# Kernel optimization log

Hardware: AMD Instinct MI355X
Metric: run time of the kernel (lower is better)

## Reference

```python
import jax, jax.numpy as jnp
import numpy as np

N = 100000        # nodes
E = 1600000       # directed edges
F = 602           # Reddit num_features
D = 32            # EMBEDDING_SIZE
C = 41            # Reddit num_classes
BN_EPS = 1e-5


def setup_inputs() -> dict:
    key = jax.random.key(0)
    ks = jax.random.split(key, 24)
    def w(k, shape, fan_in):
        return jax.random.normal(k, shape, dtype=jnp.float32) * (1.0 / np.sqrt(fan_in))
    inp = {
        "x": jax.random.normal(ks[0], (N, F), dtype=jnp.float32),
        "edge_index": jax.random.randint(ks[1], (2, E), 0, N, dtype=jnp.int32),
        # lin1: F -> 2*D
        "lin1_w": w(ks[2], (F, 2 * D), F), "lin1_b": jnp.zeros((2 * D,), jnp.float32),
        # conv1 MLP: 2*D -> D -> D
        "nn1_w1": w(ks[3], (2 * D, D), 2 * D), "nn1_b1": jnp.zeros((D,), jnp.float32),
        "nn1_w2": w(ks[4], (D, D), D), "nn1_b2": jnp.zeros((D,), jnp.float32),
        "bn1_g": jnp.ones((D,), jnp.float32), "bn1_b": jnp.zeros((D,), jnp.float32),
        # conv2 MLP: D -> D -> D
        "nn2_w1": w(ks[5], (D, D), D), "nn2_b1": jnp.zeros((D,), jnp.float32),
        "nn2_w2": w(ks[6], (D, D), D), "nn2_b2": jnp.zeros((D,), jnp.float32),
        "bn2_g": jnp.ones((D,), jnp.float32), "bn2_b": jnp.zeros((D,), jnp.float32),
        # heads
        "fc1_w": w(ks[7], (D, D), D), "fc1_b": jnp.zeros((D,), jnp.float32),
        "fc2_w": w(ks[8], (D, C), D), "fc2_b": jnp.zeros((C,), jnp.float32),
    }
    return inp


def _gin_conv(x, src, dst, w1, b1, w2, b2, eps=0.0):
    # sum-aggregate neighbor features (adj_t @ x) then MLP
    agg = jax.ops.segment_sum(x[src], dst, num_segments=N)  # [N, d]
    h = (1.0 + eps) * x + agg
    h = jnp.maximum(h @ w1 + b1, 0.0) @ w2 + b2
    return h


def _batch_norm(x, gamma, beta):
    # training-mode BatchNorm1d: batch statistics, biased variance
    mu = jnp.mean(x, axis=0)
    var = jnp.mean(jnp.square(x - mu), axis=0)
    return (x - mu) * jax.lax.rsqrt(var + BN_EPS) * gamma + beta


def reference(x, edge_index, lin1_w, lin1_b,
              nn1_w1, nn1_b1, nn1_w2, nn1_b2, bn1_g, bn1_b,
              nn2_w1, nn2_b1, nn2_w2, nn2_b2, bn2_g, bn2_b,
              fc1_w, fc1_b, fc2_w, fc2_b):
    src, dst = edge_index[0], edge_index[1]
    h = x @ lin1_w + lin1_b                                  # [N, 64]
    h = _batch_norm(_gin_conv(h, src, dst, nn1_w1, nn1_b1, nn1_w2, nn1_b2), bn1_g, bn1_b)
    h = _batch_norm(_gin_conv(h, src, dst, nn2_w1, nn2_b1, nn2_w2, nn2_b2), bn2_g, bn2_b)
    h = jnp.maximum(h @ fc1_w + fc1_b, 0.0)
    return h @ fc2_w + fc2_b                                 # [N, C]
```

## Files before the change

kernel.cpp:

```cpp
#include <hip/hip_runtime.h>
#include <cstdint>

#define NN 100000
#define NE 1600000
#define FI 602
#define DD 32
#define CC 41
#define BN_EPS 1e-5f
#define KSTEPS 19

#define NPB 256
#define NB 391
#define BST 4608
#define EPT 13
#define SCB 481

typedef __attribute__((ext_vector_type(8))) short bf16x8;
typedef __attribute__((ext_vector_type(4))) float f32x4;

__device__ __forceinline__ void atomAdd(float* p, float v) {
#ifdef __HIP_PLATFORM_AMD__
  unsafeAtomicAdd(p, v);
#else
  atomicAdd(p, v);
#endif
}

__device__ __forceinline__ unsigned short f2b(float f) {
  unsigned u = __float_as_uint(f);
  unsigned r = (u + 0x7fffu + ((u >> 16) & 1u)) >> 16;
  return (unsigned short)r;
}
__device__ __forceinline__ float blo(unsigned u) { return __uint_as_float(u << 16); }
__device__ __forceinline__ float bhi(unsigned u) { return __uint_as_float(u & 0xffff0000u); }

__global__ __launch_bounds__(256) void k0_prep(
    const float* __restrict__ lin1_w, const float* __restrict__ lin1_b,
    const float* __restrict__ nn1_w1,
    unsigned short* __restrict__ Bh,
    float* __restrict__ cvec,
    float* __restrict__ stats1, float* __restrict__ stats2) {
  int o = blockIdx.x * 256 + threadIdx.x;
  if (o < KSTEPS * 32 * 32) {
    int k = o >> 5, j = o & 31;
    float s = 0.f;
    if (k < FI) {
      #pragma unroll 4
      for (int c = 0; c < 2 * DD; ++c) s = fmaf(lin1_w[k * (2 * DD) + c], nn1_w1[c * DD + j], s);
    }
    int st = k >> 5, kk = k & 31, g = kk >> 3, jj = kk & 7;
    int h = j >> 4, lane = g * 16 + (j & 15);
    int idx = ((st * 2 + h) * 64 + lane) * 8 + jj;
    Bh[idx] = f2b(s);
  }
  if (blockIdx.x == 0) {
    int t = threadIdx.x;
    if (t < DD) {
      float s = 0.f;
      for (int c = 0; c < 2 * DD; ++c) s = fmaf(lin1_b[c], nn1_w1[c * DD + t], s);
      cvec[t] = s;
    }
    if (t >= 128 && t < 192) stats1[t - 128] = 0.f;
    if (t >= 192) stats2[t - 192] = 0.f;
  }
}

__global__ __launch_bounds__(256) void kb_scatter(const int* __restrict__ ei,
                                                  int* __restrict__ bcursor,
                                                  int* __restrict__ tsrc,
                                                  unsigned char* __restrict__ tdst) {
  __shared__ int cnt[NB];
  __shared__ int wbase[NB];
  const int t = threadIdx.x;
  for (int i = t; i < NB; i += 256) cnt[i] = 0;
  __syncthreads();
  const int base = blockIdx.x * (256 * EPT);
  int s[EPT], d[EPT];
  #pragma unroll
  for (int i = 0; i < EPT; ++i) {
    int e = base + i * 256 + t;
    if (e < NE) {
      s[i] = ei[e];
      d[i] = ei[NE + e];
      atomicAdd(&cnt[d[i] >> 8], 1);
    } else {
      s[i] = -1; d[i] = -1;
    }
  }
  __syncthreads();
  for (int i = t; i < NB; i += 256) wbase[i] = atomicAdd(&bcursor[i], cnt[i]);
  __syncthreads();
  #pragma unroll
  for (int i = 0; i < EPT; ++i) {
    if (d[i] >= 0) {
      int bk = d[i] >> 8;
      int p = atomicAdd(&wbase[bk], 1);
      int gp = bk * BST + p;
      tsrc[gp] = s[i];
      tdst[gp] = (unsigned char)(d[i] & (NPB - 1));
    }
  }
}

__global__ __launch_bounds__(256) void kb_fine(const int* __restrict__ bcursor,
                                               const int* __restrict__ tsrc,
                                               const unsigned char* __restrict__ tdst,
                                               int* __restrict__ rs, int* __restrict__ re,
                                               int* __restrict__ srcidx) {
  __shared__ int deg[NPB];
  __shared__ int cur[NPB];
  __shared__ int woff[4];
  const int b = blockIdx.x, t = threadIdx.x;
  const int beg = b * BST;
  const int end = beg + bcursor[b];
  deg[t] = 0;
  __syncthreads();
  for (int i = beg + t; i < end; i += 256) atomicAdd(&deg[tdst[i]], 1);
  __syncthreads();
  int v = deg[t];
  int lane = t & 63, wave = t >> 6;
  int inc = v;
  #pragma unroll
  for (int off = 1; off < 64; off <<= 1) {
    int u = __shfl_up(inc, off);
    if (lane >= off) inc += u;
  }
  if (lane == 63) woff[wave] = inc;
  __syncthreads();
  int wadd = 0;
  for (int w = 0; w < wave; ++w) wadd += woff[w];
  int excl = wadd + inc - v;
  int gnode = b * NPB + t;
  if (gnode < NN) {
    rs[gnode] = beg + excl;
    re[gnode] = beg + excl + v;
  }
  cur[t] = beg + excl;
  __syncthreads();
  for (int i = beg + t; i < end; i += 256) {
    int p = atomicAdd(&cur[tdst[i]], 1);
    srcidx[p] = tsrc[i];
  }
}

__global__ __launch_bounds__(256) void k1_mfma(
    const float* __restrict__ x,
    const unsigned short* __restrict__ Bh,
    const float* __restrict__ cvec, unsigned short* __restrict__ zb) {
  __shared__ float part[2][64][9];
  const int tid = threadIdx.x;
  const int lane = tid & 63;
  const int w = tid >> 6;
  const int rg = w & 1;
  const int kh = w >> 1;
  const int row0 = blockIdx.x * 32 + rg * 16;
  const int g = lane >> 4;
  const int r = row0 + (lane & 15);
  const float* __restrict__ xr = x + (size_t)r * FI + g * 8;
  f32x4 acc0 = {0.f, 0.f, 0.f, 0.f};
  f32x4 acc1 = {0.f, 0.f, 0.f, 0.f};

  if (kh == 0) {
    float4 a0 = *(const float4*)&xr[0];
    float4 b0 = *(const float4*)&xr[4];
    float4 a1 = *(const float4*)&xr[32];
    float4 b1 = *(const float4*)&xr[36];
    bf16x8 f0c = *(const bf16x8*)&Bh[(size_t)lane * 8];
    bf16x8 f1c = *(const bf16x8*)&Bh[(size_t)lane * 8 + 512];
    #pragma unroll
    for (int s = 0; s < 10; ++s) {
      float4 ca = a0, cb = b0;
      a0 = a1; b0 = b1;
      if (s + 2 < 10) {
        a1 = *(const float4*)&xr[(s + 2) * 32];
        b1 = *(const float4*)&xr[(s + 2) * 32 + 4];
      }
      bf16x8 f0n, f1n;
      if (s + 1 < 10) {
        const size_t fb = ((size_t)((s + 1) * 2) * 64 + lane) * 8;
        f0n = *(const bf16x8*)&Bh[fb];
        f1n = *(const bf16x8*)&Bh[fb + 512];
      }
      bf16x8 ahi, alo;
      float cv0[8] = {ca.x, ca.y, ca.z, ca.w, cb.x, cb.y, cb.z, cb.w};
      #pragma unroll
      for (int j = 0; j < 8; ++j) {
        unsigned ub = __float_as_uint(cv0[j]);
        unsigned short h = (unsigned short)(ub >> 16);
        float hv = __uint_as_float(ub & 0xffff0000u);
        float d = cv0[j] - hv;
        ahi[j] = (short)h;
        alo[j] = (short)(__float_as_uint(d) >> 16);
      }
      acc0 = __builtin_amdgcn_mfma_f32_16x16x32_bf16(ahi, f0c, acc0, 0, 0, 0);
      acc1 = __builtin_amdgcn_mfma_f32_16x16x32_bf16(ahi, f1c, acc1, 0, 0, 0);
      acc0 = __builtin_amdgcn_mfma_f32_16x16x32_bf16(alo, f0c, acc0, 0, 0, 0);
      acc1 = __builtin_amdgcn_mfma_f32_16x16x32_bf16(alo, f1c, acc1, 0, 0, 0);
      if (s + 1 < 10) { f0c = f0n; f1c = f1n; }
    }
  } else {
    float4 a0 = *(const float4*)&xr[10 * 32];
    float4 b0 = *(const float4*)&xr[10 * 32 + 4];
    float4 a1 = *(const float4*)&xr[11 * 32];
    float4 b1 = *(const float4*)&xr[11 * 32 + 4];
    bf16x8 f0c = *(const bf16x8*)&Bh[((size_t)(10 * 2) * 64 + lane) * 8];
    bf16x8 f1c = *(const bf16x8*)&Bh[((size_t)(10 * 2) * 64 + lane) * 8 + 512];
    #pragma unroll
    for (int s = 10; s < KSTEPS; ++s) {
      float4 ca = a0, cb = b0;
      a0 = a1; b0 = b1;
      if (s + 2 < KSTEPS - 1) {
        a1 = *(const float4*)&xr[(s + 2) * 32];
        b1 = *(const float4*)&xr[(s + 2) * 32 + 4];
      } else if (s + 2 == KSTEPS - 1) {
        if (g == 3) {
          float2 tt = *(const float2*)&xr[18 * 32];
          a1 = make_float4(tt.x, tt.y, 0.f, 0.f);
          b1 = make_float4(0.f, 0.f, 0.f, 0.f);
        } else {
          a1 = *(const float4*)&xr[18 * 32];
          b1 = *(const float4*)&xr[18 * 32 + 4];
        }
      }
      bf16x8 f0n, f1n;
      if (s + 1 < KSTEPS) {
        const size_t fb = ((size_t)((s + 1) * 2) * 64 + lane) * 8;
        f0n = *(const bf16x8*)&Bh[fb];
        f1n = *(const bf16x8*)&Bh[fb + 512];
      }
      bf16x8 ahi, alo;
      float cv0[8] = {ca.x, ca.y, ca.z, ca.w, cb.x, cb.y, cb.z, cb.w};
      #pragma unroll
      for (int j = 0; j < 8; ++j) {
        unsigned ub = __float_as_uint(cv0[j]);
        unsigned short h = (unsigned short)(ub >> 16);
        float hv = __uint_as_float(ub & 0xffff0000u);
        float d = cv0[j] - hv;
        ahi[j] = (short)h;
        alo[j] = (short)(__float_as_uint(d) >> 16);
      }
      acc0 = __builtin_amdgcn_mfma_f32_16x16x32_bf16(ahi, f0c, acc0, 0, 0, 0);
      acc1 = __builtin_amdgcn_mfma_f32_16x16x32_bf16(ahi, f1c, acc1, 0, 0, 0);
      acc0 = __builtin_amdgcn_mfma_f32_16x16x32_bf16(alo, f0c, acc0, 0, 0, 0);
      acc1 = __builtin_amdgcn_mfma_f32_16x16x32_bf16(alo, f1c, acc1, 0, 0, 0);
      if (s + 1 < KSTEPS) { f0c = f0n; f1c = f1n; }
    }
    #pragma unroll
    for (int j = 0; j < 4; ++j) {
      part[rg][lane][j] = acc0[j];
      part[rg][lane][4 + j] = acc1[j];
    }
  }
  __syncthreads();
  if (kh == 0) {
    const int c0 = lane & 15;
    const float cva = cvec[c0], cvb = cvec[16 + c0];
    #pragma unroll
    for (int j = 0; j < 4; ++j) {
      float v0 = acc0[j] + part[rg][lane][j] + cva;
      float v1 = acc1[j] + part[rg][lane][4 + j] + cvb;
      int rr = row0 + g * 4 + j;
      zb[(size_t)rr * DD + c0] = f2b(v0);
      zb[(size_t)rr * DD + 16 + c0] = f2b(v1);
    }
  }
}

__device__ __forceinline__ void gather8(const unsigned short* __restrict__ srcb,
                                        const int* __restrict__ srcidx,
                                        int beg, int end, int q, float* a) {
  int i = beg;
  for (; i + 8 <= end; i += 8) {
    uint4 v[8];
    #pragma unroll
    for (int j = 0; j < 8; ++j) v[j] = *(const uint4*)&srcb[(size_t)srcidx[i + j] * DD + q * 8];
    #pragma unroll
    for (int j = 0; j < 8; ++j) {
      a[0] += blo(v[j].x); a[1] += bhi(v[j].x);
      a[2] += blo(v[j].y); a[3] += bhi(v[j].y);
      a[4] += blo(v[j].z); a[5] += bhi(v[j].z);
      a[6] += blo(v[j].w); a[7] += bhi(v[j].w);
    }
  }
  for (; i + 4 <= end; i += 4) {
    uint4 v[4];
    #pragma unroll
    for (int j = 0; j < 4; ++j) v[j] = *(const uint4*)&srcb[(size_t)srcidx[i + j] * DD + q * 8];
    #pragma unroll
    for (int j = 0; j < 4; ++j) {
      a[0] += blo(v[j].x); a[1] += bhi(v[j].x);
      a[2] += blo(v[j].y); a[3] += bhi(v[j].y);
      a[4] += blo(v[j].z); a[5] += bhi(v[j].z);
      a[6] += blo(v[j].w); a[7] += bhi(v[j].w);
    }
  }
  for (; i < end; ++i) {
    uint4 v0 = *(const uint4*)&srcb[(size_t)srcidx[i] * DD + q * 8];
    a[0] += blo(v0.x); a[1] += bhi(v0.x);
    a[2] += blo(v0.y); a[3] += bhi(v0.y);
    a[4] += blo(v0.z); a[5] += bhi(v0.z);
    a[6] += blo(v0.w); a[7] += bhi(v0.w);
  }
}

__global__ __launch_bounds__(256) void k3_fused(
    const unsigned short* __restrict__ zb,
    const int* __restrict__ rsA, const int* __restrict__ reA,
    const int* __restrict__ srcidx,
    const float* __restrict__ w2, const float* __restrict__ b1, const float* __restrict__ b2,
    unsigned short* __restrict__ g1b, float* __restrict__ stats) {
  __shared__ float w2s[DD * DD];
  __shared__ float b1s[DD], b2s[DD];
  __shared__ float ps[4][2 * DD];
  const int tid = threadIdx.x;
  const int lane = tid & 63;
  const int q = tid & 3;
  const int n = blockIdx.x * 64 + (tid >> 2);
  const bool valid = n < NN;
  for (int i = tid; i < DD * DD; i += 256) w2s[i] = w2[i];
  if (tid < DD) b1s[tid] = b1[tid];
  else if (tid < 2 * DD) b2s[tid - DD] = b2[tid - DD];
  __syncthreads();

  float a[8] = {};
  if (valid) {
    uint4 v = *(const uint4*)&zb[(size_t)n * DD + q * 8];
    a[0] = blo(v.x); a[1] = bhi(v.x); a[2] = blo(v.y); a[3] = bhi(v.y);
    a[4] = blo(v.z); a[5] = bhi(v.z); a[6] = blo(v.w); a[7] = bhi(v.w);
    gather8(zb, srcidx, rsA[n], reA[n], q, a);
  }
  float g[8];
  #pragma unroll
  for (int j = 0; j < 8; ++j) g[j] = b2s[q * 8 + j];
  #pragma unroll
  for (int k = 0; k < DD; ++k) {
    float uv = __shfl(a[k & 7], (lane & 0x3c) | (k >> 3), 64);
    float tv = fmaxf(uv + b1s[k], 0.f);
    #pragma unroll
    for (int j = 0; j < 8; ++j) g[j] = fmaf(tv, w2s[k * DD + q * 8 + j], g[j]);
  }
  float sv[8], sq[8];
  #pragma unroll
  for (int j = 0; j < 8; ++j) { sv[j] = valid ? g[j] : 0.f; sq[j] = sv[j] * sv[j]; }
  #pragma unroll
  for (int j = 0; j < 8; ++j) {
    #pragma unroll
    for (int off = 4; off < 64; off <<= 1) { sv[j] += __shfl_xor(sv[j], off); sq[j] += __shfl_xor(sq[j], off); }
  }
  if (lane < 4) {
    int w = tid >> 6;
    #pragma unroll
    for (int j = 0; j < 8; ++j) { ps[w][q * 8 + j] = sv[j]; ps[w][DD + q * 8 + j] = sq[j]; }
  }
  if (valid) {
    unsigned u0 = ((unsigned)f2b(g[1]) << 16) | f2b(g[0]);
    unsigned u1 = ((unsigned)f2b(g[3]) << 16) | f2b(g[2]);
    unsigned u2 = ((unsigned)f2b(g[5]) << 16) | f2b(g[4]);
    unsigned u3 = ((unsigned)f2b(g[7]) << 16) | f2b(g[6]);
    *(uint4*)&g1b[(size_t)n * DD + q * 8] = make_uint4(u0, u1, u2, u3);
  }
  __syncthreads();
  if (tid < 2 * DD)
    atomAdd(&stats[tid], ps[0][tid] + ps[1][tid] + ps[2][tid] + ps[3][tid]);
}

__global__ __launch_bounds__(256) void k6_fused(
    const unsigned short* __restrict__ g1b,
    const int* __restrict__ rsA, const int* __restrict__ reA,
    const int* __restrict__ srcidx,
    const float* __restrict__ stats1, const float* __restrict__ bn1_g, const float* __restrict__ bn1_b,
    const float* __restrict__ w1, const float* __restrict__ b1,
    const float* __restrict__ w2, const float* __restrict__ b2,
    float* __restrict__ g2, float* __restrict__ stats) {
  __shared__ float w1s[DD * DD];
  __shared__ float w2s[DD * DD];
  __shared__ float bns[2 * DD];
  __shared__ float b1s[DD], b2s[DD];
  __shared__ float ps[4][2 * DD];
  const int tid = threadIdx.x;
  const int lane = tid & 63;
  const int q = tid & 3;
  const int n = blockIdx.x * 64 + (tid >> 2);
  const bool valid = n < NN;
  for (int i = tid; i < DD * DD; i += 256) { w1s[i] = w1[i]; w2s[i] = w2[i]; }
  if (tid < DD) {
    float mu = stats1[tid] * (1.f / NN);
    float var = stats1[DD + tid] * (1.f / NN) - mu * mu;
    float rsv = rsqrtf(var + BN_EPS) * bn1_g[tid];
    bns[tid] = rsv;
    bns[DD + tid] = bn1_b[tid] - mu * rsv;
    b1s[tid] = b1[tid];
  } else if (tid < 2 * DD) {
    b2s[tid - DD] = b2[tid - DD];
  }
  __syncthreads();

  float a[8] = {};
  float degp1 = 1.f;
  if (valid) {
    uint4 v = *(const uint4*)&g1b[(size_t)n * DD + q * 8];
    a[0] = blo(v.x); a[1] = bhi(v.x); a[2] = blo(v.y); a[3] = bhi(v.y);
    a[4] = blo(v.z); a[5] = bhi(v.z); a[6] = blo(v.w); a[7] = bhi(v.w);
    int beg = rsA[n], end = reA[n];
    degp1 = (float)(end - beg + 1);
    gather8(g1b, srcidx, beg, end, q, a);
  }
  float t1[8];
  #pragma unroll
  for (int j = 0; j < 8; ++j) t1[j] = b1s[q * 8 + j];
  #pragma unroll
  for (int k = 0; k < DD; ++k) {
    float uv = __shfl(a[k & 7], (lane & 0x3c) | (k >> 3), 64);
    float u = fmaf(uv, bns[k], degp1 * bns[DD + k]);
    #pragma unroll
    for (int j = 0; j < 8; ++j) t1[j] = fmaf(u, w1s[k * DD + q * 8 + j], t1[j]);
  }
  #pragma unroll
  for (int j = 0; j < 8; ++j) t1[j] = fmaxf(t1[j], 0.f);
  float g[8];
  #pragma unroll
  for (int j = 0; j < 8; ++j) g[j] = b2s[q * 8 + j];
  #pragma unroll
  for (int k = 0; k < DD; ++k) {
    float tv = __shfl(t1[k & 7], (lane & 0x3c) | (k >> 3), 64);
    #pragma unroll
    for (int j = 0; j < 8; ++j) g[j] = fmaf(tv, w2s[k * DD + q * 8 + j], g[j]);
  }
  float sv[8], sq[8];
  #pragma unroll
  for (int j = 0; j < 8; ++j) { sv[j] = valid ? g[j] : 0.f; sq[j] = sv[j] * sv[j]; }
  #pragma unroll
  for (int j = 0; j < 8; ++j) {
    #pragma unroll
    for (int off = 4; off < 64; off <<= 1) { sv[j] += __shfl_xor(sv[j], off); sq[j] += __shfl_xor(sq[j], off); }
  }
  if (lane < 4) {
    int w = tid >> 6;
    #pragma unroll
    for (int j = 0; j < 8; ++j) { ps[w][q * 8 + j] = sv[j]; ps[w][DD + q * 8 + j] = sq[j]; }
  }
  if (valid) {
    float* gp = &g2[(size_t)n * DD + q * 8];
    *(float4*)&gp[0] = make_float4(g[0], g[1], g[2], g[3]);
    *(float4*)&gp[4] = make_float4(g[4], g[5], g[6], g[7]);
  }
  __syncthreads();
  if (tid < 2 * DD)
    atomAdd(&stats[tid], ps[0][tid] + ps[1][tid] + ps[2][tid] + ps[3][tid]);
}

__global__ __launch_bounds__(256) void k7_head(
    const float* __restrict__ g2, const float* __restrict__ stats2,
    const float* __restrict__ bn2_g, const float* __restrict__ bn2_b,
    const float* __restrict__ fc1_w, const float* __restrict__ fc1_b,
    const float* __restrict__ fc2_w, const float* __restrict__ fc2_b,
    float* __restrict__ out) {
  __shared__ float buf[256 * 42];
  __shared__ float fc1s[DD * DD];
  __shared__ float fc2s[DD * CC];
  __shared__ float mu2[DD], rsg2[DD], bet2[DD];
  const int tid = threadIdx.x;
  const int n0 = blockIdx.x * 256;
  if (tid < DD) {
    float mu = stats2[tid] * (1.f / NN);
    float var = stats2[DD + tid] * (1.f / NN) - mu * mu;
    mu2[tid] = mu;
    rsg2[tid] = rsqrtf(var + BN_EPS) * bn2_g[tid];
    bet2[tid] = bn2_b[tid];
  }
  for (int i = tid; i < DD * DD; i += 256) fc1s[i] = fc1_w[i];
  for (int i = tid; i < DD * CC; i += 256) fc2s[i] = fc2_w[i];
  __syncthreads();
  #pragma unroll
  for (int i = 0; i < 32; ++i) {
    int l = tid + i * 256;
    int r = l >> 5, c = l & 31;
    float v = 0.f;
    if (n0 + r < NN) v = (g2[(size_t)(n0 + r) * DD + c] - mu2[c]) * rsg2[c] + bet2[c];
    buf[r * 33 + c] = v;
  }
  __syncthreads();
  float t[DD];
  #pragma unroll
  for (int j = 0; j < DD; ++j) t[j] = fc1_b[j];
  #pragma unroll
  for (int k = 0; k < DD; ++k) {
    float uv = buf[tid * 33 + k];
    #pragma unroll
    for (int j = 0; j < DD; ++j) t[j] = fmaf(uv, fc1s[k * DD + j], t[j]);
  }
  #pragma unroll
  for (int j = 0; j < DD; ++j) t[j] = fmaxf(t[j], 0.f);
  float o[CC];
  #pragma unroll
  for (int j = 0; j < CC; ++j) o[j] = fc2_b[j];
  #pragma unroll
  for (int k = 0; k < DD; ++k) {
    float tv = t[k];
    #pragma unroll
    for (int j = 0; j < CC; ++j) o[j] = fmaf(tv, fc2s[k * CC + j], o[j]);
  }
  __syncthreads();
  #pragma unroll
  for (int j = 0; j < CC; ++j) buf[tid * 42 + j] = o[j];
  __syncthreads();
  for (int i = 0; i < CC; ++i) {
    int l = tid + i * 256;
    int r = l / CC, c = l % CC;
    if (n0 + r < NN) out[(size_t)(n0 + r) * CC + c] = buf[r * 42 + c];
  }
}

extern "C" void kernel_launch(void* const* d_in, const int* in_sizes, int n_in,
                              void* d_out, int out_size, void* d_ws, size_t ws_size,
                              hipStream_t stream) {
  const float* x      = (const float*)d_in[0];
  const int*   ei     = (const int*)d_in[1];
  const float* lin1_w = (const float*)d_in[2];
  const float* lin1_b = (const float*)d_in[3];
  const float* nn1_w1 = (const float*)d_in[4];
  const float* nn1_b1 = (const float*)d_in[5];
  const float* nn1_w2 = (const float*)d_in[6];
  const float* nn1_b2 = (const float*)d_in[7];
  const float* bn1_g  = (const float*)d_in[8];
  const float* bn1_b  = (const float*)d_in[9];
  const float* nn2_w1 = (const float*)d_in[10];
  const float* nn2_b1 = (const float*)d_in[11];
  const float* nn2_w2 = (const float*)d_in[12];
  const float* nn2_b2 = (const float*)d_in[13];
  const float* bn2_g  = (const float*)d_in[14];
  const float* bn2_b  = (const float*)d_in[15];
  const float* fc1_w  = (const float*)d_in[16];
  const float* fc1_b  = (const float*)d_in[17];
  const float* fc2_w  = (const float*)d_in[18];
  const float* fc2_b  = (const float*)d_in[19];
  float* out = (float*)d_out;

  float* ws = (float*)d_ws;
  size_t nd = (size_t)NN * DD;
  float* A      = ws;
  float* B      = ws + nd;
  float* cvec   = ws + 2 * nd;
  float* stats1 = cvec + 32;
  float* stats2 = stats1 + 64;
  unsigned short* Bh = (unsigned short*)(stats2 + 64);
  int*   rsA      = (int*)(Bh + KSTEPS * 2 * 64 * 8);
  int*   reA      = rsA + NN;
  int*   srcidx   = reA + NN;
  int*   tsrc     = srcidx + (size_t)NB * BST;
  unsigned char* tdst = (unsigned char*)(tsrc + (size_t)NB * BST);
  int*   bcursor  = (int*)(tdst + (size_t)NB * BST);
  unsigned short* zb  = (unsigned short*)tsrc;
  unsigned short* g1b = (unsigned short*)B;

  hipMemsetAsync(bcursor, 0, NB * sizeof(int), stream);
  kb_scatter<<<SCB, 256, 0, stream>>>(ei, bcursor, tsrc, tdst);
  kb_fine<<<NB, 256, 0, stream>>>(bcursor, tsrc, tdst, rsA, reA, srcidx);

  k0_prep<<<(KSTEPS * 32 * 32 + 255) / 256, 256, 0, stream>>>(
      lin1_w, lin1_b, nn1_w1, Bh, cvec, stats1, stats2);
  k1_mfma<<<NN / 32, 256, 0, stream>>>(x, Bh, cvec, zb);
  k3_fused<<<(NN + 63) / 64, 256, 0, stream>>>(zb, rsA, reA, srcidx,
                                               nn1_w2, nn1_b1, nn1_b2, g1b, stats1);
  k6_fused<<<(NN + 63) / 64, 256, 0, stream>>>(g1b, rsA, reA, srcidx,
                                               stats1, bn1_g, bn1_b,
                                               nn2_w1, nn2_b1, nn2_w2, nn2_b2, A, stats2);
  k7_head<<<(NN + 255) / 256, 256, 0, stream>>>(A, stats2, bn2_g, bn2_b, fc1_w, fc1_b, fc2_w, fc2_b, out);
}
```

Measured before the change: 254.4 us.

## Merge prep into scatter launch, widen gather to 12, store layer-2 output as bf16

The weight-prep work now runs as extra blocks inside the edge-scatter kernel, which removes one launch and lets the two overlap. The neighbor gather is unrolled to 12 loads in flight instead of 8, to get more memory-level parallelism. The second conv output is stored as bf16 instead of fp32, halving its write and the head kernel's read. The bf16 rounding adds precision loss, and the wider unroll may raise register pressure and send more nodes down the tail loop.

```diff
diff --git a/kernel.cpp b/kernel.cpp
--- a/kernel.cpp
+++ b/kernel.cpp
@@ -14,6 +14,7 @@
 #define BST 4608
 #define EPT 13
 #define SCB 481
+#define K0B 76
 
 typedef __attribute__((ext_vector_type(8))) short bf16x8;
 typedef __attribute__((ext_vector_type(4))) float f32x4;
@@ -34,70 +35,68 @@
 __device__ __forceinline__ float blo(unsigned u) { return __uint_as_float(u << 16); }
 __device__ __forceinline__ float bhi(unsigned u) { return __uint_as_float(u & 0xffff0000u); }
 
-__global__ __launch_bounds__(256) void k0_prep(
+__global__ __launch_bounds__(256) void k0s(
+    const int* __restrict__ ei, int* __restrict__ bcursor,
+    int* __restrict__ tsrc, unsigned char* __restrict__ tdst,
     const float* __restrict__ lin1_w, const float* __restrict__ lin1_b,
     const float* __restrict__ nn1_w1,
-    unsigned short* __restrict__ Bh,
-    float* __restrict__ cvec,
+    unsigned short* __restrict__ Bh, float* __restrict__ cvec,
     float* __restrict__ stats1, float* __restrict__ stats2) {
-  int o = blockIdx.x * 256 + threadIdx.x;
-  if (o < KSTEPS * 32 * 32) {
-    int k = o >> 5, j = o & 31;
-    float s = 0.f;
-    if (k < FI) {
-      #pragma unroll 4
-      for (int c = 0; c < 2 * DD; ++c) s = fmaf(lin1_w[k * (2 * DD) + c], nn1_w1[c * DD + j], s);
-    }
-    int st = k >> 5, kk = k & 31, g = kk >> 3, jj = kk & 7;
-    int h = j >> 4, lane = g * 16 + (j & 15);
-    int idx = ((st * 2 + h) * 64 + lane) * 8 + jj;
-    Bh[idx] = f2b(s);
-  }
-  if (blockIdx.x == 0) {
-    int t = threadIdx.x;
-    if (t < DD) {
-      float s = 0.f;
-      for (int c = 0; c < 2 * DD; ++c) s = fmaf(lin1_b[c], nn1_w1[c * DD + t], s);
-      cvec[t] = s;
-    }
-    if (t >= 128 && t < 192) stats1[t - 128] = 0.f;
-    if (t >= 192) stats2[t - 192] = 0.f;
-  }
-}
-
-__global__ __launch_bounds__(256) void kb_scatter(const int* __restrict__ ei,
-                                                  int* __restrict__ bcursor,
-                                                  int* __restrict__ tsrc,
-                                                  unsigned char* __restrict__ tdst) {
   __shared__ int cnt[NB];
   __shared__ int wbase[NB];
   const int t = threadIdx.x;
-  for (int i = t; i < NB; i += 256) cnt[i] = 0;
-  __syncthreads();
-  const int base = blockIdx.x * (256 * EPT);
-  int s[EPT], d[EPT];
-  #pragma unroll
-  for (int i = 0; i < EPT; ++i) {
-    int e = base + i * 256 + t;
-    if (e < NE) {
-      s[i] = ei[e];
-      d[i] = ei[NE + e];
-      atomicAdd(&cnt[d[i] >> 8], 1);
-    } else {
-      s[i] = -1; d[i] = -1;
-    }
-  }
-  __syncthreads();
-  for (int i = t; i < NB; i += 256) wbase[i] = atomicAdd(&bcursor[i], cnt[i]);
-  __syncthreads();
-  #pragma unroll
-  for (int i = 0; i < EPT; ++i) {
-    if (d[i] >= 0) {
-      int bk = d[i] >> 8;
-      int p = atomicAdd(&wbase[bk], 1);
-      int gp = bk * BST + p;
-      tsrc[gp] = s[i];
-      tdst[gp] = (unsigned char)(d[i] & (NPB - 1));
+  const int blk = blockIdx.x;
+  if (blk < SCB) {
+    for (int i = t; i < NB; i += 256) cnt[i] = 0;
+    __syncthreads();
+    const int base = blk * (256 * EPT);
+    int s[EPT], d[EPT];
+    #pragma unroll
+    for (int i = 0; i < EPT; ++i) {
+      int e = base + i * 256 + t;
+      if (e < NE) {
+        s[i] = ei[e];
+        d[i] = ei[NE + e];
+        atomicAdd(&cnt[d[i] >> 8], 1);
+      } else {
+        s[i] = -1; d[i] = -1;
+      }
+    }
+    __syncthreads();
+    for (int i = t; i < NB; i += 256) wbase[i] = atomicAdd(&bcursor[i], cnt[i]);
+    __syncthreads();
+    #pragma unroll
+    for (int i = 0; i < EPT; ++i) {
+      if (d[i] >= 0) {
+        int bk = d[i] >> 8;
+        int p = atomicAdd(&wbase[bk], 1);
+        int gp = bk * BST + p;
+        tsrc[gp] = s[i];
+        tdst[gp] = (unsigned char)(d[i] & (NPB - 1));
+      }
+    }
+  } else {
+    int o = (blk - SCB) * 256 + t;
+    if (o < KSTEPS * 32 * 32) {
+      int k = o >> 5, j = o & 31;
+      float sm = 0.f;
+      if (k < FI) {
+        #pragma unroll 4
+        for (int c = 0; c < 2 * DD; ++c) sm = fmaf(lin1_w[k * (2 * DD) + c], nn1_w1[c * DD + j], sm);
+      }
+      int st = k >> 5, kk = k & 31, g = kk >> 3, jj = kk & 7;
+      int h = j >> 4, lane = g * 16 + (j & 15);
+      int idx = ((st * 2 + h) * 64 + lane) * 8 + jj;
+      Bh[idx] = f2b(sm);
+    }
+    if (blk == SCB) {
+      if (t < DD) {
+        float sm = 0.f;
+        for (int c = 0; c < 2 * DD; ++c) sm = fmaf(lin1_b[c], nn1_w1[c * DD + t], sm);
+        cvec[t] = sm;
+      }
+      if (t >= 128 && t < 192) stats1[t - 128] = 0.f;
+      if (t >= 192) stats2[t - 192] = 0.f;
     }
   }
 }
@@ -266,16 +265,16 @@
   }
 }
 
-__device__ __forceinline__ void gather8(const unsigned short* __restrict__ srcb,
-                                        const int* __restrict__ srcidx,
-                                        int beg, int end, int q, float* a) {
+__device__ __forceinline__ void gather12(const unsigned short* __restrict__ srcb,
+                                         const int* __restrict__ srcidx,
+                                         int beg, int end, int q, float* a) {
   int i = beg;
-  for (; i + 8 <= end; i += 8) {
-    uint4 v[8];
-    #pragma unroll
-    for (int j = 0; j < 8; ++j) v[j] = *(const uint4*)&srcb[(size_t)srcidx[i + j] * DD + q * 8];
-    #pragma unroll
-    for (int j = 0; j < 8; ++j) {
+  for (; i + 12 <= end; i += 12) {
+    uint4 v[12];
+    #pragma unroll
+    for (int j = 0; j < 12; ++j) v[j] = *(const uint4*)&srcb[(size_t)srcidx[i + j] * DD + q * 8];
+    #pragma unroll
+    for (int j = 0; j < 12; ++j) {
       a[0] += blo(v[j].x); a[1] += bhi(v[j].x);
       a[2] += blo(v[j].y); a[3] += bhi(v[j].y);
       a[4] += blo(v[j].z); a[5] += bhi(v[j].z);
@@ -327,7 +326,7 @@
     uint4 v = *(const uint4*)&zb[(size_t)n * DD + q * 8];
     a[0] = blo(v.x); a[1] = bhi(v.x); a[2] = blo(v.y); a[3] = bhi(v.y);
     a[4] = blo(v.z); a[5] = bhi(v.z); a[6] = blo(v.w); a[7] = bhi(v.w);
-    gather8(zb, srcidx, rsA[n], reA[n], q, a);
+    gather12(zb, srcidx, rsA[n], reA[n], q, a);
   }
   float g[8];
   #pragma unroll
@@ -371,7 +370,7 @@
     const float* __restrict__ stats1, const float* __restrict__ bn1_g, const float* __restrict__ bn1_b,
     const float* __restrict__ w1, const float* __restrict__ b1,
     const float* __restrict__ w2, const float* __restrict__ b2,
-    float* __restrict__ g2, float* __restrict__ stats) {
+    unsigned short* __restrict__ g2b, float* __restrict__ stats) {
   __shared__ float w1s[DD * DD];
   __shared__ float w2s[DD * DD];
   __shared__ float bns[2 * DD];
@@ -403,7 +402,7 @@
     a[4] = blo(v.z); a[5] = bhi(v.z); a[6] = blo(v.w); a[7] = bhi(v.w);
     int beg = rsA[n], end = reA[n];
     degp1 = (float)(end - beg + 1);
-    gather8(g1b, srcidx, beg, end, q, a);
+    gather12(g1b, srcidx, beg, end, q, a);
   }
   float t1[8];
   #pragma unroll
@@ -440,9 +439,11 @@
     for (int j = 0; j < 8; ++j) { ps[w][q * 8 + j] = sv[j]; ps[w][DD + q * 8 + j] = sq[j]; }
   }
   if (valid) {
-    float* gp = &g2[(size_t)n * DD + q * 8];
-    *(float4*)&gp[0] = make_float4(g[0], g[1], g[2], g[3]);
-    *(float4*)&gp[4] = make_float4(g[4], g[5], g[6], g[7]);
+    unsigned u0 = ((unsigned)f2b(g[1]) << 16) | f2b(g[0]);
+    unsigned u1 = ((unsigned)f2b(g[3]) << 16) | f2b(g[2]);
+    unsigned u2 = ((unsigned)f2b(g[5]) << 16) | f2b(g[4]);
+    unsigned u3 = ((unsigned)f2b(g[7]) << 16) | f2b(g[6]);
+    *(uint4*)&g2b[(size_t)n * DD + q * 8] = make_uint4(u0, u1, u2, u3);
   }
   __syncthreads();
   if (tid < 2 * DD)
@@ -450,7 +451,7 @@
 }
 
 __global__ __launch_bounds__(256) void k7_head(
-    const float* __restrict__ g2, const float* __restrict__ stats2,
+    const unsigned short* __restrict__ g2b, const float* __restrict__ stats2,
     const float* __restrict__ bn2_g, const float* __restrict__ bn2_b,
     const float* __restrict__ fc1_w, const float* __restrict__ fc1_b,
     const float* __restrict__ fc2_w, const float* __restrict__ fc2_b,
@@ -472,12 +473,17 @@
   for (int i = tid; i < DD * CC; i += 256) fc2s[i] = fc2_w[i];
   __syncthreads();
   #pragma unroll
-  for (int i = 0; i < 32; ++i) {
+  for (int i = 0; i < 16; ++i) {
     int l = tid + i * 256;
-    int r = l >> 5, c = l & 31;
-    float v = 0.f;
-    if (n0 + r < NN) v = (g2[(size_t)(n0 + r) * DD + c] - mu2[c]) * rsg2[c] + bet2[c];
-    buf[r * 33 + c] = v;
+    int r = l >> 4, c2 = l & 15;
+    float lo = 0.f, hi = 0.f;
+    if (n0 + r < NN) {
+      unsigned u = *(const unsigned*)&g2b[(size_t)(n0 + r) * DD + c2 * 2];
+      lo = (blo(u) - mu2[c2 * 2]) * rsg2[c2 * 2] + bet2[c2 * 2];
+      hi = (bhi(u) - mu2[c2 * 2 + 1]) * rsg2[c2 * 2 + 1] + bet2[c2 * 2 + 1];
+    }
+    buf[r * 33 + c2 * 2] = lo;
+    buf[r * 33 + c2 * 2 + 1] = hi;
   }
   __syncthreads();
   float t[DD];
@@ -552,18 +558,18 @@
   int*   bcursor  = (int*)(tdst + (size_t)NB * BST);
   unsigned short* zb  = (unsigned short*)tsrc;
   unsigned short* g1b = (unsigned short*)B;
+  unsigned short* g2b = (unsigned short*)A;
 
   hipMemsetAsync(bcursor, 0, NB * sizeof(int), stream);
-  kb_scatter<<<SCB, 256, 0, stream>>>(ei, bcursor, tsrc, tdst);
+  k0s<<<SCB + K0B, 256, 0, stream>>>(ei, bcursor, tsrc, tdst,
+                                     lin1_w, lin1_b, nn1_w1, Bh, cvec, stats1, stats2);
   kb_fine<<<NB, 256, 0, stream>>>(bcursor, tsrc, tdst, rsA, reA, srcidx);
-
-  k0_prep<<<(KSTEPS * 32 * 32 + 255) / 256, 256, 0, stream>>>(
-      lin1_w, lin1_b, nn1_w1, Bh, cvec, stats1, stats2);
   k1_mfma<<<NN / 32, 256, 0, stream>>>(x, Bh, cvec, zb);
   k3_fused<<<(NN + 63) / 64, 256, 0, stream>>>(zb, rsA, reA, srcidx,
                                                nn1_w2, nn1_b1, nn1_b2, g1b, stats1);
   k6_fused<<<(NN + 63) / 64, 256, 0, stream>>>(g1b, rsA, reA, srcidx,
                                                stats1, bn1_g, bn1_b,
-                                               nn2_w1, nn2_b1, nn2_w2, nn2_b2, A, stats2);
-  k7_head<<<(NN + 255) / 256, 256, 0, stream>>>(A, stats2, bn2_g, bn2_b, fc1_w, fc1_b, fc2_w, fc2_b, out);
-}
+                                               nn2_w1, nn2_b1, nn2_w2, nn2_b2, g2b, stats2);
+  k7_head<<<(NN + 255) / 256, 256, 0, stream>>>(g2b, stats2, bn2_g, bn2_b,
+                                                fc1_w, fc1_b, fc2_w, fc2_b, out);
+}
```

Measured after the change: 240.7 us. 5.4% less time.
